# Optimization experiments

Measured on AMD Instinct MI355X. Metric: run time of the kernel, lower is better.

## Reference

```python
import jax, jax.numpy as jnp
import numpy as np

E = 800_000   # number of scattered elements (edges)
Q = 50_000    # number of queries (segments)
D = 128       # in_embed_dim == in_queries_dim == qk_proj_dim


def setup_inputs() -> dict:
    key = jax.random.key(0)
    k_sv, k_idx, k_q, k_wq, k_bq, k_wk, k_bk = jax.random.split(key, 7)
    lim = 1.0 / np.sqrt(D)
    return {
        "scattered_values": jax.random.normal(k_sv, (E, D), dtype=jnp.float32),
        "indices": jax.random.randint(k_idx, (E,), 0, Q, dtype=jnp.int32),
        "queries": jax.random.normal(k_q, (Q, D), dtype=jnp.float32),
        "Wq": jax.random.uniform(k_wq, (D, D), jnp.float32, -lim, lim),
        "bq": jax.random.uniform(k_bq, (D,), jnp.float32, -lim, lim),
        "Wk": jax.random.uniform(k_wk, (D, D), jnp.float32, -lim, lim),
        "bk": jax.random.uniform(k_bk, (D,), jnp.float32, -lim, lim),
    }


def reference(scattered_values, indices, queries, Wq, bq, Wk, bk):
    num_segments = queries.shape[0]
    proj_dim = Wq.shape[1]

    # Project queries [Q, P] then gather per element -> [E, P]
    q_proj = queries @ Wq + bq
    q_gathered = q_proj[indices]

    # Project keys [E, P]
    keys = scattered_values @ Wk + bk

    # Per-element dot-product scores, scaled
    scale = proj_dim ** (-0.5)
    probs = jnp.einsum("ed,ed->e", keys, q_gathered) * scale  # [E]

    # Segment (scatter) softmax over elements sharing the same index
    seg_max = jax.ops.segment_max(probs, indices, num_segments=num_segments)
    ex = jnp.exp(probs - seg_max[indices])
    seg_sum = jax.ops.segment_sum(ex, indices, num_segments=num_segments)
    scores = ex / seg_sum[indices]  # [E]

    # Weighted scatter-sum of (unprojected) values -> [Q, D]
    attn_applied = jax.ops.segment_sum(
        scattered_values * scores[:, None], indices, num_segments=num_segments
    )
    return scores, attn_applied
```

## Files before the change

### kernel.cpp

```cpp
#include <hip/hip_runtime.h>
#include <math.h>

#define DD 128

__global__ void k_init(const float* __restrict__ Wq, const float* __restrict__ bq,
                       const float* __restrict__ Wk, const float* __restrict__ bk,
                       float* __restrict__ M, float* __restrict__ tvec,
                       float* __restrict__ uvec, float* __restrict__ s0,
                       int* __restrict__ hist, int* __restrict__ done,
                       int Q, int NB) {
    const int tid = threadIdx.x;
    if (blockIdx.x < (unsigned)NB) {
        int base = blockIdx.x * 256;
        for (int j = base + tid; j < base + 256; j += 128)
            if (j < Q) hist[j] = 0;
        if (blockIdx.x == 0 && tid == 0) *done = 0;
        return;
    }
    __shared__ float wkT[64][129];
    __shared__ float wqrow[128];
    __shared__ float bqs[128];
    const int dp = blockIdx.x - NB;
    wqrow[tid] = Wq[dp * DD + tid];
    bqs[tid]   = bq[tid];
    float acc = 0.f, tacc = 0.f;
    for (int ch = 0; ch < 2; ++ch) {
        __syncthreads();
        for (int i = tid; i < 128 * 64; i += 128) {
            int d = i >> 6, j = i & 63;
            wkT[j][d] = Wk[d * DD + ch * 64 + j];
        }
        __syncthreads();
        #pragma unroll 8
        for (int j = 0; j < 64; ++j) {
            float w = wkT[j][tid];
            acc  += wqrow[ch * 64 + j] * w;
            tacc += bqs[ch * 64 + j] * w;
        }
    }
    M[dp * DD + tid] = acc;
    if (dp == 0) {
        tvec[tid] = tacc;
        float ua = 0.f;
        for (int p = 0; p < DD; ++p) ua += Wq[tid * DD + p] * bk[p];
        uvec[tid] = ua;
        if (tid == 0) {
            float s = 0.f;
            for (int p = 0; p < DD; ++p) s += bq[p] * bk[p];
            *s0 = s;
        }
    }
}

__global__ __launch_bounds__(256) void k_gemm(const float* __restrict__ queries,
                                              const float* __restrict__ M,
                                              const float* __restrict__ tvec,
                                              float* __restrict__ zs, int Q, float scale) {
    __shared__ __align__(16) float Ms[32 * 128];
    __shared__ float qs[64 * 33];
    const int t  = threadIdx.x;
    const int tx = t & 15;
    const int ty = t >> 4;
    const int qbase = blockIdx.x * 64;
    float acc[4][8];
    #pragma unroll
    for (int j = 0; j < 4; ++j)
        #pragma unroll
        for (int i = 0; i < 8; ++i) acc[j][i] = 0.f;

    for (int kc = 0; kc < 4; ++kc) {
        __syncthreads();
        for (int i = t; i < 1024; i += 256) {
            int r = i >> 5, c4 = i & 31;
            ((float4*)Ms)[r * 32 + c4] = ((const float4*)(M + (size_t)(kc * 32 + r) * DD))[c4];
        }
        for (int i = t; i < 2048; i += 256) {
            int r = i >> 5, c = i & 31;
            int q = qbase + r;
            qs[r * 33 + c] = (q < Q) ? queries[(size_t)q * DD + kc * 32 + c] : 0.f;
        }
        __syncthreads();
        #pragma unroll 8
        for (int k = 0; k < 32; ++k) {
            float4 ma = *(const float4*)&Ms[k * 128 + tx * 8];
            float4 mb = *(const float4*)&Ms[k * 128 + tx * 8 + 4];
            float mv[8] = {ma.x, ma.y, ma.z, ma.w, mb.x, mb.y, mb.z, mb.w};
            #pragma unroll
            for (int j = 0; j < 4; ++j) {
                float qv = qs[(ty * 4 + j) * 33 + k];
                #pragma unroll
                for (int i = 0; i < 8; ++i) acc[j][i] = fmaf(qv, mv[i], acc[j][i]);
            }
        }
    }
    float4 t0 = *(const float4*)(tvec + tx * 8);
    float4 t1 = *(const float4*)(tvec + tx * 8 + 4);
    float tv[8] = {t0.x, t0.y, t0.z, t0.w, t1.x, t1.y, t1.z, t1.w};
    #pragma unroll
    for (int j = 0; j < 4; ++j) {
        int q = qbase + ty * 4 + j;
        if (q < Q) {
            float o[8];
            #pragma unroll
            for (int i = 0; i < 8; ++i) o[i] = (acc[j][i] + tv[i]) * scale;
            float4 w0 = {o[0], o[1], o[2], o[3]};
            float4 w1 = {o[4], o[5], o[6], o[7]};
            *(float4*)(zs + (size_t)q * DD + tx * 8)     = w0;
            *(float4*)(zs + (size_t)q * DD + tx * 8 + 4) = w1;
        }
    }
}

__global__ void k_hist(const int* __restrict__ idx, int* __restrict__ hist, int E) {
    int i = blockIdx.x * blockDim.x + threadIdx.x;
    if (i < E) atomicAdd(&hist[idx[i]], 1);
}

__global__ void k_scan12(const int* __restrict__ hist, int* __restrict__ bsum,
                         int* __restrict__ boff, int* __restrict__ done,
                         int Q, int NB) {
    const int t = threadIdx.x;
    int i = blockIdx.x * 256 + t;
    int v = (i < Q) ? hist[i] : 0;
    #pragma unroll
    for (int off = 1; off < 64; off <<= 1) v += __shfl_xor(v, off);
    __shared__ int sd[4];
    __shared__ int ticket;
    if ((t & 63) == 0) sd[t >> 6] = v;
    __syncthreads();
    if (t == 0) {
        bsum[blockIdx.x] = sd[0] + sd[1] + sd[2] + sd[3];
        __threadfence();
        ticket = atomicAdd(done, 1);
    }
    __syncthreads();
    if (ticket == NB - 1) {
        __threadfence();
        __shared__ int s[256];
        int vv = (t < NB) ? bsum[t] : 0;
        s[t] = vv;
        __syncthreads();
        for (int off = 1; off < 256; off <<= 1) {
            int add = (t >= off) ? s[t - off] : 0;
            __syncthreads();
            s[t] += add;
            __syncthreads();
        }
        if (t < NB) boff[t] = s[t] - vv;
    }
}

__global__ void k_scan3(const int* __restrict__ hist, const int* __restrict__ boff,
                        int* __restrict__ seg_start, int* __restrict__ cursor, int Q) {
    __shared__ int s[256];
    int t = threadIdx.x;
    int i = blockIdx.x * 256 + t;
    int v = (i < Q) ? hist[i] : 0;
    s[t] = v;
    __syncthreads();
    for (int off = 1; off < 256; off <<= 1) {
        int add = (t >= off) ? s[t - off] : 0;
        __syncthreads();
        s[t] += add;
        __syncthreads();
    }
    if (i < Q) {
        int excl = s[t] - v + boff[blockIdx.x];
        seg_start[i] = excl;
        cursor[i]    = excl;
    }
}

__global__ void k_scatter(const int* __restrict__ idx, int* __restrict__ cursor,
                          int* __restrict__ perm, int E) {
    int i = blockIdx.x * blockDim.x + threadIdx.x;
    if (i < E) {
        int q   = idx[i];
        int pos = atomicAdd(&cursor[q], 1);
        perm[pos] = i;
    }
}

__global__ __launch_bounds__(256) void k_attn(const float* __restrict__ SV,
                                              const float* __restrict__ queries,
                                              const float* __restrict__ uvec,
                                              const float* __restrict__ s0ptr,
                                              const int* __restrict__ hist,
                                              const int* __restrict__ seg_start,
                                              const int* __restrict__ perm,
                                              float* __restrict__ zs_attn,
                                              float* __restrict__ scores,
                                              float* __restrict__ invsum,
                                              int Q, float scale) {
    const int wid  = threadIdx.x >> 6;
    const int lane = threadIdx.x & 63;
    const int q    = blockIdx.x * 4 + wid;
    if (q >= Q) return;

    float2 zv  = ((const float2*)(zs_attn + (size_t)q * DD))[lane];
    float2 qv2 = ((const float2*)(queries + (size_t)q * DD))[lane];
    float2 uv2 = ((const float2*)uvec)[lane];
    float cd = fmaf(qv2.x, uv2.x, qv2.y * uv2.y);
    #pragma unroll
    for (int off = 1; off < 64; off <<= 1) cd += __shfl_xor(cd, off);
    const float cq = (cd + s0ptr[0]) * scale;

    const int cnt   = hist[q];
    const int start = seg_start[q];

    float accx = 0.f, accy = 0.f, ssum = 0.f;
    for (int base = 0; base < cnt; base += 64) {
        const int m = min(64, cnt - base);
        int pe = perm[start + base + ((lane < m) ? lane : 0)];
        for (int i = 0; i < m; i += 4) {
            const int i1 = min(i + 1, m - 1);
            const int i2 = min(i + 2, m - 1);
            const int i3 = min(i + 3, m - 1);
            const int e0 = __shfl(pe, i);
            const int e1 = __shfl(pe, i1);
            const int e2 = __shfl(pe, i2);
            const int e3 = __shfl(pe, i3);
            const float2 s0v = ((const float2*)(SV + (size_t)e0 * DD))[lane];
            const float2 s1v = ((const float2*)(SV + (size_t)e1 * DD))[lane];
            const float2 s2v = ((const float2*)(SV + (size_t)e2 * DD))[lane];
            const float2 s3v = ((const float2*)(SV + (size_t)e3 * DD))[lane];
            float p0 = fmaf(s0v.x, zv.x, s0v.y * zv.y);
            float p1 = fmaf(s1v.x, zv.x, s1v.y * zv.y);
            float p2 = fmaf(s2v.x, zv.x, s2v.y * zv.y);
            float p3 = fmaf(s3v.x, zv.x, s3v.y * zv.y);
            #pragma unroll
            for (int off = 1; off < 64; off <<= 1) {
                p0 += __shfl_xor(p0, off);
                p1 += __shfl_xor(p1, off);
                p2 += __shfl_xor(p2, off);
                p3 += __shfl_xor(p3, off);
            }
            const float ex0 = __expf(p0 + cq);
            const float ex1 = (i + 1 < m) ? __expf(p1 + cq) : 0.f;
            const float ex2 = (i + 2 < m) ? __expf(p2 + cq) : 0.f;
            const float ex3 = (i + 3 < m) ? __expf(p3 + cq) : 0.f;
            ssum += (ex0 + ex1) + (ex2 + ex3);
            accx = fmaf(ex0, s0v.x, fmaf(ex1, s1v.x, fmaf(ex2, s2v.x, fmaf(ex3, s3v.x, accx))));
            accy = fmaf(ex0, s0v.y, fmaf(ex1, s1v.y, fmaf(ex2, s2v.y, fmaf(ex3, s3v.y, accy))));
            if (lane == 0) {
                scores[e0] = ex0;
                if (i + 1 < m) scores[e1] = ex1;
                if (i + 2 < m) scores[e2] = ex2;
                if (i + 3 < m) scores[e3] = ex3;
            }
        }
    }

    float2* arow = (float2*)(zs_attn + (size_t)q * DD);
    if (cnt == 0) {
        arow[lane] = make_float2(0.f, 0.f);
    } else {
        const float inv = 1.f / ssum;
        arow[lane] = make_float2(accx * inv, accy * inv);
        if (lane == 0) invsum[q] = inv;
    }
}

__global__ void k_rescale(const int* __restrict__ idx, const float* __restrict__ invsum,
                          float* __restrict__ scores, int E) {
    int i = blockIdx.x * blockDim.x + threadIdx.x;
    if (i < E) scores[i] = scores[i] * invsum[idx[i]];
}

extern "C" void kernel_launch(void* const* d_in, const int* in_sizes, int n_in,
                              void* d_out, int out_size, void* d_ws, size_t ws_size,
                              hipStream_t stream) {
    const float* SV      = (const float*)d_in[0];
    const int*   indices = (const int*)d_in[1];
    const float* queries = (const float*)d_in[2];
    const float* Wq      = (const float*)d_in[3];
    const float* bq      = (const float*)d_in[4];
    const float* Wk      = (const float*)d_in[5];
    const float* bk      = (const float*)d_in[6];

    const int E = in_sizes[1];
    const int Q = in_sizes[2] / DD;
    const float scale = 1.0f / sqrtf((float)DD);

    float* scores  = (float*)d_out;
    float* zs_attn = (float*)d_out + E;

    float* ws   = (float*)d_ws;
    float* M    = ws;
    float* tvec = ws + 16384;
    float* uvec = ws + 16512;
    float* s0   = ws + 16640;
    int* hist      = (int*)ws + 17024;
    int* seg_start = hist + Q;
    int* cursor    = seg_start + Q;
    int* bsum      = cursor + Q;
    int* boff      = bsum + 256;
    int* done      = boff + 256;
    int* perm      = done + 64;
    float* invsum  = (float*)(perm + E);

    const int NB = (Q + 255) / 256;

    hipLaunchKernelGGL(k_init, dim3(NB + 128), dim3(128), 0, stream,
                       Wq, bq, Wk, bk, M, tvec, uvec, s0, hist, done, Q, NB);
    hipLaunchKernelGGL(k_gemm, dim3((Q + 63) / 64), dim3(256), 0, stream,
                       queries, M, tvec, zs_attn, Q, scale);
    hipLaunchKernelGGL(k_hist, dim3((E + 255) / 256), dim3(256), 0, stream,
                       indices, hist, E);
    hipLaunchKernelGGL(k_scan12, dim3(NB), dim3(256), 0, stream,
                       hist, bsum, boff, done, Q, NB);
    hipLaunchKernelGGL(k_scan3, dim3(NB), dim3(256), 0, stream,
                       hist, boff, seg_start, cursor, Q);
    hipLaunchKernelGGL(k_scatter, dim3((E + 255) / 256), dim3(256), 0, stream,
                       indices, cursor, perm, E);
    hipLaunchKernelGGL(k_attn, dim3((Q + 3) / 4), dim3(256), 0, stream,
                       SV, queries, uvec, s0, hist, seg_start, perm,
                       zs_attn, scores, invsum, Q, scale);
    hipLaunchKernelGGL(k_rescale, dim3((E + 255) / 256), dim3(256), 0, stream,
                       indices, invsum, scores, E);
}
```

Baseline: 737.1 us.

## Fuse histogram into GEMM launch, widen attn loads, write scores in sorted order

Merges the histogram kernel into the GEMM launch as extra blocks, so the two run concurrently and one launch is saved. The attention kernel now has each half-wave load a full float4 row slice, which processes two elements per shuffle-reduction step with a shorter 32-lane reduction. Exponentials are stored contiguously in segment-sorted order rather than scattered across scores, and an inverse-position array lets the rescale pass gather them back. This trades scattered writes in attention for an extra E-sized int write in scatter plus a gather in rescale.

Measured after the change: 717.4 us. -2.7%, faster.

```diff
diff --git a/kernel.cpp b/kernel.cpp
--- a/kernel.cpp
+++ b/kernel.cpp
@@ -52,10 +52,17 @@
     }
 }
 
-__global__ __launch_bounds__(256) void k_gemm(const float* __restrict__ queries,
-                                              const float* __restrict__ M,
-                                              const float* __restrict__ tvec,
-                                              float* __restrict__ zs, int Q, float scale) {
+__global__ __launch_bounds__(256) void k_gemm_hist(const float* __restrict__ queries,
+                                                   const float* __restrict__ M,
+                                                   const float* __restrict__ tvec,
+                                                   float* __restrict__ zs, int Q, float scale,
+                                                   const int* __restrict__ idx,
+                                                   int* __restrict__ hist, int E, int GB) {
+    if (blockIdx.x >= (unsigned)GB) {
+        int i = (blockIdx.x - GB) * 256 + threadIdx.x;
+        if (i < E) atomicAdd(&hist[idx[i]], 1);
+        return;
+    }
     __shared__ __align__(16) float Ms[32 * 128];
     __shared__ float qs[64 * 33];
     const int t  = threadIdx.x;
@@ -109,11 +116,6 @@
             *(float4*)(zs + (size_t)q * DD + tx * 8 + 4) = w1;
         }
     }
-}
-
-__global__ void k_hist(const int* __restrict__ idx, int* __restrict__ hist, int E) {
-    int i = blockIdx.x * blockDim.x + threadIdx.x;
-    if (i < E) atomicAdd(&hist[idx[i]], 1);
 }
 
 __global__ void k_scan12(const int* __restrict__ hist, int* __restrict__ bsum,
@@ -172,12 +174,13 @@
 }
 
 __global__ void k_scatter(const int* __restrict__ idx, int* __restrict__ cursor,
-                          int* __restrict__ perm, int E) {
+                          int* __restrict__ perm, int* __restrict__ inv_pos, int E) {
     int i = blockIdx.x * blockDim.x + threadIdx.x;
     if (i < E) {
         int q   = idx[i];
         int pos = atomicAdd(&cursor[q], 1);
-        perm[pos] = i;
+        perm[pos]  = i;
+        inv_pos[i] = pos;
     }
 }
 
@@ -189,15 +192,18 @@
                                               const int* __restrict__ seg_start,
                                               const int* __restrict__ perm,
                                               float* __restrict__ zs_attn,
-                                              float* __restrict__ scores,
+                                              float* __restrict__ ex_sorted,
                                               float* __restrict__ invsum,
                                               int Q, float scale) {
     const int wid  = threadIdx.x >> 6;
     const int lane = threadIdx.x & 63;
     const int q    = blockIdx.x * 4 + wid;
     if (q >= Q) return;
-
-    float2 zv  = ((const float2*)(zs_attn + (size_t)q * DD))[lane];
+    const int half = lane >> 5;
+    const int col4 = lane & 31;
+
+    const float4 zv = ((const float4*)(zs_attn + (size_t)q * DD))[col4];
+
     float2 qv2 = ((const float2*)(queries + (size_t)q * DD))[lane];
     float2 uv2 = ((const float2*)uvec)[lane];
     float cd = fmaf(qv2.x, uv2.x, qv2.y * uv2.y);
@@ -208,63 +214,76 @@
     const int cnt   = hist[q];
     const int start = seg_start[q];
 
-    float accx = 0.f, accy = 0.f, ssum = 0.f;
+    float4 acc = make_float4(0.f, 0.f, 0.f, 0.f);
+    float ssum = 0.f;
+
     for (int base = 0; base < cnt; base += 64) {
         const int m = min(64, cnt - base);
-        int pe = perm[start + base + ((lane < m) ? lane : 0)];
-        for (int i = 0; i < m; i += 4) {
-            const int i1 = min(i + 1, m - 1);
-            const int i2 = min(i + 2, m - 1);
-            const int i3 = min(i + 3, m - 1);
-            const int e0 = __shfl(pe, i);
-            const int e1 = __shfl(pe, i1);
-            const int e2 = __shfl(pe, i2);
-            const int e3 = __shfl(pe, i3);
-            const float2 s0v = ((const float2*)(SV + (size_t)e0 * DD))[lane];
-            const float2 s1v = ((const float2*)(SV + (size_t)e1 * DD))[lane];
-            const float2 s2v = ((const float2*)(SV + (size_t)e2 * DD))[lane];
-            const float2 s3v = ((const float2*)(SV + (size_t)e3 * DD))[lane];
-            float p0 = fmaf(s0v.x, zv.x, s0v.y * zv.y);
-            float p1 = fmaf(s1v.x, zv.x, s1v.y * zv.y);
-            float p2 = fmaf(s2v.x, zv.x, s2v.y * zv.y);
-            float p3 = fmaf(s3v.x, zv.x, s3v.y * zv.y);
-            #pragma unroll
-            for (int off = 1; off < 64; off <<= 1) {
-                p0 += __shfl_xor(p0, off);
-                p1 += __shfl_xor(p1, off);
-                p2 += __shfl_xor(p2, off);
-                p3 += __shfl_xor(p3, off);
-            }
-            const float ex0 = __expf(p0 + cq);
-            const float ex1 = (i + 1 < m) ? __expf(p1 + cq) : 0.f;
-            const float ex2 = (i + 2 < m) ? __expf(p2 + cq) : 0.f;
-            const float ex3 = (i + 3 < m) ? __expf(p3 + cq) : 0.f;
-            ssum += (ex0 + ex1) + (ex2 + ex3);
-            accx = fmaf(ex0, s0v.x, fmaf(ex1, s1v.x, fmaf(ex2, s2v.x, fmaf(ex3, s3v.x, accx))));
-            accy = fmaf(ex0, s0v.y, fmaf(ex1, s1v.y, fmaf(ex2, s2v.y, fmaf(ex3, s3v.y, accy))));
-            if (lane == 0) {
-                scores[e0] = ex0;
-                if (i + 1 < m) scores[e1] = ex1;
-                if (i + 2 < m) scores[e2] = ex2;
-                if (i + 3 < m) scores[e3] = ex3;
-            }
-        }
-    }
-
-    float2* arow = (float2*)(zs_attn + (size_t)q * DD);
+        const int pe = perm[start + base + ((lane < m) ? lane : 0)];
+        for (int i = 0; i < m; i += 8) {
+            int   rr[4], valid[4];
+            float4 sv[4];
+            #pragma unroll
+            for (int j = 0; j < 4; ++j) {
+                rr[j]   = i + 2 * j + half;
+                valid[j] = (rr[j] < m);
+                int r   = valid[j] ? rr[j] : (m - 1);
+                int e   = __shfl(pe, r);
+                sv[j]   = ((const float4*)(SV + (size_t)e * DD))[col4];
+            }
+            float p[4];
+            #pragma unroll
+            for (int j = 0; j < 4; ++j)
+                p[j] = fmaf(sv[j].x, zv.x, fmaf(sv[j].y, zv.y,
+                        fmaf(sv[j].z, zv.z, sv[j].w * zv.w)));
+            #pragma unroll
+            for (int off = 1; off < 32; off <<= 1) {
+                p[0] += __shfl_xor(p[0], off);
+                p[1] += __shfl_xor(p[1], off);
+                p[2] += __shfl_xor(p[2], off);
+                p[3] += __shfl_xor(p[3], off);
+            }
+            float ex[4];
+            #pragma unroll
+            for (int j = 0; j < 4; ++j) {
+                ex[j] = valid[j] ? __expf(p[j] + cq) : 0.f;
+                ssum += ex[j];
+                acc.x = fmaf(ex[j], sv[j].x, acc.x);
+                acc.y = fmaf(ex[j], sv[j].y, acc.y);
+                acc.z = fmaf(ex[j], sv[j].z, acc.z);
+                acc.w = fmaf(ex[j], sv[j].w, acc.w);
+            }
+            if (col4 == 0) {
+                #pragma unroll
+                for (int j = 0; j < 4; ++j)
+                    if (valid[j]) ex_sorted[start + base + rr[j]] = ex[j];
+            }
+        }
+    }
+
+    acc.x += __shfl_xor(acc.x, 32);
+    acc.y += __shfl_xor(acc.y, 32);
+    acc.z += __shfl_xor(acc.z, 32);
+    acc.w += __shfl_xor(acc.w, 32);
+    ssum  += __shfl_xor(ssum, 32);
+
+    float4* arow = (float4*)(zs_attn + (size_t)q * DD);
     if (cnt == 0) {
-        arow[lane] = make_float2(0.f, 0.f);
+        if (half == 0) arow[col4] = make_float4(0.f, 0.f, 0.f, 0.f);
     } else {
         const float inv = 1.f / ssum;
-        arow[lane] = make_float2(accx * inv, accy * inv);
+        if (half == 0)
+            arow[col4] = make_float4(acc.x * inv, acc.y * inv, acc.z * inv, acc.w * inv);
         if (lane == 0) invsum[q] = inv;
     }
 }
 
-__global__ void k_rescale(const int* __restrict__ idx, const float* __restrict__ invsum,
+__global__ void k_rescale(const int* __restrict__ idx, const int* __restrict__ inv_pos,
+                          const float* __restrict__ ex_sorted,
+                          const float* __restrict__ invsum,
                           float* __restrict__ scores, int E) {
     int i = blockIdx.x * blockDim.x + threadIdx.x;
-    if (i < E) scores[i] = scores[i] * invsum[idx[i]];
+    if (i < E) scores[i] = ex_sorted[inv_pos[i]] * invsum[idx[i]];
 }
 
 extern "C" void kernel_launch(void* const* d_in, const int* in_sizes, int n_in,
@@ -297,25 +316,27 @@
     int* boff      = bsum + 256;
     int* done      = boff + 256;
     int* perm      = done + 64;
-    float* invsum  = (float*)(perm + E);
+    int* inv_pos   = perm + E;
+    float* ex_sorted = (float*)(inv_pos + E);
+    float* invsum    = ex_sorted + E;
 
     const int NB = (Q + 255) / 256;
+    const int GB = (Q + 63) / 64;
+    const int HB = (E + 255) / 256;
 
     hipLaunchKernelGGL(k_init, dim3(NB + 128), dim3(128), 0, stream,
                        Wq, bq, Wk, bk, M, tvec, uvec, s0, hist, done, Q, NB);
-    hipLaunchKernelGGL(k_gemm, dim3((Q + 63) / 64), dim3(256), 0, stream,
-                       queries, M, tvec, zs_attn, Q, scale);
-    hipLaunchKernelGGL(k_hist, dim3((E + 255) / 256), dim3(256), 0, stream,
-                       indices, hist, E);
+    hipLaunchKernelGGL(k_gemm_hist, dim3(GB + HB), dim3(256), 0, stream,
+                       queries, M, tvec, zs_attn, Q, scale, indices, hist, E, GB);
     hipLaunchKernelGGL(k_scan12, dim3(NB), dim3(256), 0, stream,
                        hist, bsum, boff, done, Q, NB);
     hipLaunchKernelGGL(k_scan3, dim3(NB), dim3(256), 0, stream,
                        hist, boff, seg_start, cursor, Q);
-    hipLaunchKernelGGL(k_scatter, dim3((E + 255) / 256), dim3(256), 0, stream,
-                       indices, cursor, perm, E);
+    hipLaunchKernelGGL(k_scatter, dim3(HB), dim3(256), 0, stream,
+                       indices, cursor, perm, inv_pos, E);
     hipLaunchKernelGGL(k_attn, dim3((Q + 3) / 4), dim3(256), 0, stream,
                        SV, queries, uvec, s0, hist, seg_start, perm,
-                       zs_attn, scores, invsum, Q, scale);
-    hipLaunchKernelGGL(k_rescale, dim3((E + 255) / 256), dim3(256), 0, stream,
-                       indices, invsum, scores, E);
-}
+                       zs_attn, ex_sorted, invsum, Q, scale);
+    hipLaunchKernelGGL(k_rescale, dim3(HB), dim3(256), 0, stream,
+                       indices, inv_pos, ex_sorted, invsum, scores, E);
+}
```
